# Kernel tuning notes

Hardware: AMD Instinct MI355X
Metric: run time of the kernel (lower is better)

## Reference

```python
import jax, jax.numpy as jnp
import numpy as np

VOCAB = 256
PAD = 0
D_MODEL = 512
ATTN_DIM = 64
B, L = 8, 2048
LN_EPS = 1e-5


def layer_norm(x, g, b):
    mu = jnp.mean(x, axis=-1, keepdims=True)
    var = jnp.mean(jnp.square(x - mu), axis=-1, keepdims=True)
    return (x - mu) * jax.lax.rsqrt(var + LN_EPS) * g + b


def setup_inputs() -> dict:
    key = jax.random.key(0)
    ks = jax.random.split(key, 10)
    tokens = jax.random.randint(ks[0], (B, L), 1, VOCAB)  # avoid PAD=0
    prefix_lens = jax.random.randint(ks[1], (B,), 256, 1536)
    embed_w = jax.random.normal(ks[2], (VOCAB, D_MODEL), jnp.float32) * 0.02
    embed_w = embed_w.at[PAD].set(0.0)  # padding_idx row
    en_g = jnp.ones((D_MODEL,), jnp.float32)
    en_b = jnp.zeros((D_MODEL,), jnp.float32)
    fn_g = jnp.ones((D_MODEL,), jnp.float32)
    fn_b = jnp.zeros((D_MODEL,), jnp.float32)
    q_w = jax.random.normal(ks[3], (ATTN_DIM, D_MODEL), jnp.float32) * 0.02
    q_b = jnp.zeros((ATTN_DIM,), jnp.float32)
    k_w = jax.random.normal(ks[4], (ATTN_DIM, D_MODEL), jnp.float32) * 0.02
    k_b = jnp.zeros((ATTN_DIM,), jnp.float32)
    g_w = jax.random.normal(ks[5], (1, D_MODEL), jnp.float32) * 0.02
    g_b = jnp.full((1,), 2.0, jnp.float32)  # gate bias init to 2.0
    return dict(tokens=tokens, prefix_lens=prefix_lens, embed_w=embed_w,
                en_g=en_g, en_b=en_b, fn_g=fn_g, fn_b=fn_b,
                q_w=q_w, q_b=q_b, k_w=k_w, k_b=k_b, g_w=g_w, g_b=g_b)


def reference(tokens, prefix_lens, embed_w, en_g, en_b, fn_g, fn_b,
              q_w, q_b, k_w, k_b, g_w, g_b):
    # encode (n_layers=0: embed -> embed_norm -> final_norm)
    x = embed_w[tokens]                       # (B, L, D)
    x = layer_norm(x, en_g, en_b)
    h = layer_norm(x, fn_g, fn_b)

    vocab_logits = jnp.einsum('bld,vd->blv', h, embed_w)   # tied head
    q = h @ q_w.T + q_b                       # (B, L, A)
    k = h @ k_w.T + k_b                       # (B, L, A)
    scores = jnp.einsum('btd,bsd->bts', q, k) / np.sqrt(ATTN_DIM).astype(np.float32)

    idx = jnp.arange(L)[None, :]              # (1, L)
    prefix_mask = (idx < prefix_lens[:, None]) & (tokens != PAD)  # (B, L)
    scores = jnp.where(prefix_mask[:, None, :], scores, -jnp.inf)
    attn = jax.nn.softmax(scores, axis=-1)    # (B, L, L)

    prefix_onehot = jax.nn.one_hot(tokens, VOCAB, dtype=jnp.float32)
    prefix_onehot = prefix_onehot * prefix_mask[..., None]
    copy_dist = jnp.einsum('bts,bsv->btv', attn, prefix_onehot)  # (B, L, V)

    gate = jax.nn.sigmoid(h @ g_w.T + g_b)    # (B, L, 1)
    vocab_probs = jax.nn.softmax(vocab_logits, axis=-1)
    mixed = gate * vocab_probs + (1.0 - gate) * copy_dist
    mixed = jnp.clip(mixed, 1e-12, None)
    return jnp.log(mixed), gate[..., 0], attn
```

## Files before the change

### kernel.cpp

```cpp
#include <hip/hip_runtime.h>
#include <math.h>


#define DM 512
#define VC 256
#define SL 2048
#define NB 8
#define AD 64

typedef float f4v __attribute__((ext_vector_type(4)));

__device__ __forceinline__ float wave_sum(float v) {
#pragma unroll
  for (int o = 32; o > 0; o >>= 1) v += __shfl_xor(v, o, 64);
  return v;
}
__device__ __forceinline__ float wave_max(float v) {
#pragma unroll
  for (int o = 32; o > 0; o >>= 1) v = fmaxf(v, __shfl_xor(v, o, 64));
  return v;
}
__device__ __forceinline__ float blk_sum(float v, float* red) {
  v = wave_sum(v);
  if ((threadIdx.x & 63) == 0) red[threadIdx.x >> 6] = v;
  __syncthreads();
  float r = red[0] + red[1] + red[2] + red[3];
  __syncthreads();
  return r;
}
__device__ __forceinline__ float blk_max(float v, float* red) {
  v = wave_max(v);
  if ((threadIdx.x & 63) == 0) red[threadIdx.x >> 6] = v;
  __syncthreads();
  float r = fmaxf(fmaxf(red[0], red[1]), fmaxf(red[2], red[3]));
  __syncthreads();
  return r;
}

__global__ __launch_bounds__(256) void kprep(
    const float* __restrict__ embed_w, const float* __restrict__ q_w,
    const float* __restrict__ k_w, const int* __restrict__ tokens,
    const int* __restrict__ prefix_lens,
    float* __restrict__ embed_P, float* __restrict__ qk_P,
    int* __restrict__ cnt)
{
  __shared__ int c[VC];
  const int blk = blockIdx.x;
  const int tid = threadIdx.x;
  if (blk < DM) {
    const int d = blk;
    embed_P[(((d >> 2) * VC + tid) << 2) + (d & 3)] = embed_w[tid * DM + d];
    if (tid < 128) {
      float val = (tid < 64) ? q_w[tid * DM + d] : k_w[(tid - 64) * DM + d];
      qk_P[(((d >> 2) * 128 + tid) << 2) + (d & 3)] = val;
    }
  } else {
    const int b = blk - DM;
    c[tid] = 0;
    __syncthreads();
    const int P = prefix_lens[b];
    const int4* trow = (const int4*)(tokens + b * SL);
#pragma unroll
    for (int i = tid; i < SL / 4; i += 256) {
      int4 tk = trow[i];
      int s0 = i * 4;
      if (s0     < P && tk.x != 0) atomicAdd(&c[tk.x], 1);
      if (s0 + 1 < P && tk.y != 0) atomicAdd(&c[tk.y], 1);
      if (s0 + 2 < P && tk.z != 0) atomicAdd(&c[tk.z], 1);
      if (s0 + 3 < P && tk.w != 0) atomicAdd(&c[tk.w], 1);
    }
    __syncthreads();
    cnt[b * VC + tid] = c[tid];
  }
}

__global__ __launch_bounds__(256) void ktok(
    const float* __restrict__ embed_w,
    const float* __restrict__ en_g, const float* __restrict__ en_b,
    const float* __restrict__ fn_g, const float* __restrict__ fn_b,
    const float* __restrict__ q_b, const float* __restrict__ k_b,
    const float* __restrict__ g_w, const float* __restrict__ g_b,
    const float* __restrict__ embed_P, const float* __restrict__ qk_P,
    float* __restrict__ q_tok, float* __restrict__ kT_P,
    float* __restrict__ gate_tok, float* __restrict__ probs_tok)
{
  __shared__ float red[4];
  __shared__ __align__(16) float hs[DM];
  const int tt = blockIdx.x;
  const int tid = threadIdx.x;

  float x0 = embed_w[tt * DM + tid];
  float x1 = embed_w[tt * DM + 256 + tid];
  float mu = blk_sum(x0 + x1, red) * (1.0f / DM);
  float d0 = x0 - mu, d1 = x1 - mu;
  float var = blk_sum(d0 * d0 + d1 * d1, red) * (1.0f / DM);
  float inv = 1.0f / sqrtf(var + 1e-5f);
  float y0 = d0 * inv * en_g[tid] + en_b[tid];
  float y1 = d1 * inv * en_g[tid + 256] + en_b[tid + 256];
  mu = blk_sum(y0 + y1, red) * (1.0f / DM);
  d0 = y0 - mu; d1 = y1 - mu;
  var = blk_sum(d0 * d0 + d1 * d1, red) * (1.0f / DM);
  inv = 1.0f / sqrtf(var + 1e-5f);
  float h0 = d0 * inv * fn_g[tid] + fn_b[tid];
  float h1 = d1 * inv * fn_g[tid + 256] + fn_b[tid + 256];
  hs[tid] = h0; hs[tid + 256] = h1;
  float gp = blk_sum(h0 * g_w[tid] + h1 * g_w[tid + 256], red);
  if (tid == 0) gate_tok[tt] = 1.0f / (1.0f + expf(-(gp + g_b[0])));

  const float4* hs4 = (const float4*)hs;
  const float4* w4p = (const float4*)qk_P;
  const float4* e4p = (const float4*)embed_P;
  const bool qk_lane = (tid < 128);
  float acc = 0.0f;
  float lt = 0.0f;
#pragma unroll 8
  for (int d4 = 0; d4 < DM / 4; ++d4) {
    float4 h4 = hs4[d4];
    float4 e4 = e4p[d4 * VC + tid];
    lt += h4.x * e4.x + h4.y * e4.y + h4.z * e4.z + h4.w * e4.w;
    if (qk_lane) {
      float4 w4 = w4p[d4 * 128 + tid];
      acc += h4.x * w4.x + h4.y * w4.y + h4.z * w4.z + h4.w * w4.w;
    }
  }
  if (qk_lane) {
    if (tid < 64) {
      q_tok[tt * AD + tid] = acc + q_b[tid];
    } else {
      int a = tid - 64;
      kT_P[(((a >> 2) * VC + tt) << 2) + (a & 3)] = acc + k_b[a];
    }
  }
  float m = blk_max(lt, red);
  float e = expf(lt - m);
  float Z = blk_sum(e, red);
  probs_tok[tt * VC + tid] = e / Z;
}

__global__ __launch_bounds__(256) void ktables(
    const float* __restrict__ q_tok, const float* __restrict__ kT_P,
    const int* __restrict__ cnt, const float* __restrict__ gate_tok,
    const float* __restrict__ probs_tok,
    float* __restrict__ e_norm, float* __restrict__ logmix)
{
  __shared__ float red[4];
  __shared__ __align__(16) float qs[AD];
  const int b = blockIdx.x >> 8, tt = blockIdx.x & 255;
  const int v = threadIdx.x;
  if (v < AD) qs[v] = q_tok[tt * AD + v];
  __syncthreads();
  const float4* qs4 = (const float4*)qs;
  const float4* k4p = (const float4*)kT_P;
  float sv = 0.0f;
#pragma unroll
  for (int a4 = 0; a4 < AD / 4; ++a4) {
    float4 q4 = qs4[a4];
    float4 k4 = k4p[a4 * VC + v];
    sv += q4.x * k4.x + q4.y * k4.y + q4.z * k4.z + q4.w * k4.w;
  }
  sv *= 0.125f;
  int c = cnt[b * VC + v];
  float m = blk_max(c > 0 ? sv : -1e30f, red);
  float e = expf(sv - m);
  float Z = blk_sum((float)c * e, red);
  float en = e / Z;
  int idx = (b * VC + tt) * VC + v;
  e_norm[idx] = en;
  float g = gate_tok[tt];
  float mixed = g * probs_tok[tt * VC + v] + (1.0f - g) * ((float)c * en);
  logmix[idx] = logf(fmaxf(mixed, 1e-12f));
}

__global__ __launch_bounds__(256) void kwrite(
    const int* __restrict__ tokens, const int* __restrict__ prefix_lens,
    const float* __restrict__ e_norm, const float* __restrict__ logmix,
    const float* __restrict__ gate_tok,
    float* __restrict__ out_logmix, float* __restrict__ out_gate,
    float* __restrict__ out_attn)
{
  __shared__ float erow[VC];
  const int row = blockIdx.x;
  const int b = row >> 11;
  const int tid = threadIdx.x;
  const int P = prefix_lens[b];
  const int4* tokrow = (const int4*)(tokens + b * SL);
  int4 tk0 = tokrow[tid];
  int4 tk1 = tokrow[tid + 256];
  const int tt = tokens[row];
  const int base = (b * VC + tt) * VC;
  erow[tid] = e_norm[base + tid];
  __builtin_nontemporal_store(logmix[base + tid],
                              &out_logmix[(size_t)row * VC + tid]);
  if (tid == 0) out_gate[row] = gate_tok[tt];
  __syncthreads();
  f4v* arow = (f4v*)(out_attn + (size_t)row * SL);
  {
    int s0 = tid * 4;
    f4v val;
    val.x = (s0     < P && tk0.x != 0) ? erow[tk0.x] : 0.0f;
    val.y = (s0 + 1 < P && tk0.y != 0) ? erow[tk0.y] : 0.0f;
    val.z = (s0 + 2 < P && tk0.z != 0) ? erow[tk0.z] : 0.0f;
    val.w = (s0 + 3 < P && tk0.w != 0) ? erow[tk0.w] : 0.0f;
    __builtin_nontemporal_store(val, &arow[tid]);
  }
  {
    int s0 = (tid + 256) * 4;
    f4v val;
    val.x = (s0     < P && tk1.x != 0) ? erow[tk1.x] : 0.0f;
    val.y = (s0 + 1 < P && tk1.y != 0) ? erow[tk1.y] : 0.0f;
    val.z = (s0 + 2 < P && tk1.z != 0) ? erow[tk1.z] : 0.0f;
    val.w = (s0 + 3 < P && tk1.w != 0) ? erow[tk1.w] : 0.0f;
    __builtin_nontemporal_store(val, &arow[tid + 256]);
  }
}

extern "C" void kernel_launch(void* const* d_in, const int* in_sizes, int n_in,
                              void* d_out, int out_size, void* d_ws, size_t ws_size,
                              hipStream_t stream)
{
  const int*   tokens      = (const int*)  d_in[0];
  const int*   prefix_lens = (const int*)  d_in[1];
  const float* embed_w     = (const float*)d_in[2];
  const float* en_g        = (const float*)d_in[3];
  const float* en_b        = (const float*)d_in[4];
  const float* fn_g        = (const float*)d_in[5];
  const float* fn_b        = (const float*)d_in[6];
  const float* q_b         = (const float*)d_in[8];
  const float* k_b         = (const float*)d_in[10];
  const float* q_w         = (const float*)d_in[7];
  const float* k_w         = (const float*)d_in[9];
  const float* g_w         = (const float*)d_in[11];
  const float* g_b         = (const float*)d_in[12];

  float* ws        = (float*)d_ws;
  float* embed_P   = ws;
  float* qk_P      = embed_P + DM * VC;
  float* kT_P      = qk_P + DM * 128;
  float* q_tok     = kT_P + AD * VC;
  float* gate_tok  = q_tok + VC * AD;
  float* probs_tok = gate_tok + VC;
  int*   cnt       = (int*)(probs_tok + VC * VC);
  float* e_norm    = (float*)(cnt + NB * VC);
  float* logmix    = e_norm + NB * VC * VC;

  float* out_logmix = (float*)d_out;
  float* out_gate   = out_logmix + (size_t)NB * SL * VC;
  float* out_attn   = out_gate + (size_t)NB * SL;

  kprep<<<DM + NB, 256, 0, stream>>>(embed_w, q_w, k_w, tokens, prefix_lens,
                                     embed_P, qk_P, cnt);
  ktok<<<VC, 256, 0, stream>>>(embed_w, en_g, en_b, fn_g, fn_b, q_b, k_b,
                               g_w, g_b, embed_P, qk_P,
                               q_tok, kT_P, gate_tok, probs_tok);
  ktables<<<NB * VC, 256, 0, stream>>>(q_tok, kT_P, cnt, gate_tok, probs_tok,
                                       e_norm, logmix);
  kwrite<<<NB * SL, 256, 0, stream>>>(tokens, prefix_lens, e_norm, logmix,
                                      gate_tok, out_logmix, out_gate, out_attn);
}
```

Measured before the change: 239.8 us.

## Fuse table and write kernels via per-token row lists built by counting sort

kprep now also counts every token occurrence per batch, prefix-sums the counts and scatters row positions into per-(batch,token) lists. A single fused kernel per (batch, token) computes the attention and log-mix rows once, then writes them directly to every output row holding that token. This removes the e_norm/logmix workspace round-trip and a separate 16K-block launch. Write work is now unevenly spread across blocks according to token frequency, and output writes are scattered rather than sequential.

Result: no change. 238.5 us, median of 2 (-0.5%).

```diff
diff --git a/kernel.cpp b/kernel.cpp
--- a/kernel.cpp
+++ b/kernel.cpp
@@ -42,9 +42,13 @@
     const float* __restrict__ k_w, const int* __restrict__ tokens,
     const int* __restrict__ prefix_lens,
     float* __restrict__ embed_P, float* __restrict__ qk_P,
-    int* __restrict__ cnt)
+    int* __restrict__ cnt, int* __restrict__ ncnt,
+    int* __restrict__ offs, int* __restrict__ list)
 {
   __shared__ int c[VC];
+  __shared__ int ca[VC];
+  __shared__ int off[VC];
+  __shared__ int cur[VC];
   const int blk = blockIdx.x;
   const int tid = threadIdx.x;
   if (blk < DM) {
@@ -56,7 +60,7 @@
     }
   } else {
     const int b = blk - DM;
-    c[tid] = 0;
+    c[tid] = 0; ca[tid] = 0;
     __syncthreads();
     const int P = prefix_lens[b];
     const int4* trow = (const int4*)(tokens + b * SL);
@@ -64,13 +68,40 @@
     for (int i = tid; i < SL / 4; i += 256) {
       int4 tk = trow[i];
       int s0 = i * 4;
+      atomicAdd(&ca[tk.x], 1); atomicAdd(&ca[tk.y], 1);
+      atomicAdd(&ca[tk.z], 1); atomicAdd(&ca[tk.w], 1);
       if (s0     < P && tk.x != 0) atomicAdd(&c[tk.x], 1);
       if (s0 + 1 < P && tk.y != 0) atomicAdd(&c[tk.y], 1);
       if (s0 + 2 < P && tk.z != 0) atomicAdd(&c[tk.z], 1);
       if (s0 + 3 < P && tk.w != 0) atomicAdd(&c[tk.w], 1);
     }
     __syncthreads();
-    cnt[b * VC + tid] = c[tid];
+    int myc = ca[tid];
+    off[tid] = myc;
+    __syncthreads();
+    for (int d2 = 1; d2 < VC; d2 <<= 1) {
+      int add = (tid >= d2) ? off[tid - d2] : 0;
+      __syncthreads();
+      off[tid] += add;
+      __syncthreads();
+    }
+    int excl = off[tid] - myc;
+    cur[tid] = excl;
+    __syncthreads();
+#pragma unroll
+    for (int i = tid; i < SL / 4; i += 256) {
+      int4 tk = trow[i];
+      int s0 = i * 4;
+      int p;
+      p = atomicAdd(&cur[tk.x], 1); list[b * SL + p] = s0;
+      p = atomicAdd(&cur[tk.y], 1); list[b * SL + p] = s0 + 1;
+      p = atomicAdd(&cur[tk.z], 1); list[b * SL + p] = s0 + 2;
+      p = atomicAdd(&cur[tk.w], 1); list[b * SL + p] = s0 + 3;
+    }
+    __syncthreads();
+    cnt [b * VC + tid] = c[tid];
+    ncnt[b * VC + tid] = myc;
+    offs[b * VC + tid] = excl;
   }
 }
 
@@ -137,80 +168,76 @@
   probs_tok[tt * VC + tid] = e / Z;
 }
 
-__global__ __launch_bounds__(256) void ktables(
+__global__ __launch_bounds__(256) void kfused(
     const float* __restrict__ q_tok, const float* __restrict__ kT_P,
-    const int* __restrict__ cnt, const float* __restrict__ gate_tok,
-    const float* __restrict__ probs_tok,
-    float* __restrict__ e_norm, float* __restrict__ logmix)
+    const int* __restrict__ cnt, const int* __restrict__ ncnt,
+    const int* __restrict__ offs, const int* __restrict__ list,
+    const float* __restrict__ gate_tok, const float* __restrict__ probs_tok,
+    const int* __restrict__ tokens, const int* __restrict__ prefix_lens,
+    float* __restrict__ out_logmix, float* __restrict__ out_gate,
+    float* __restrict__ out_attn)
 {
   __shared__ float red[4];
   __shared__ __align__(16) float qs[AD];
+  __shared__ __align__(16) float erow[VC];
   const int b = blockIdx.x >> 8, tt = blockIdx.x & 255;
-  const int v = threadIdx.x;
-  if (v < AD) qs[v] = q_tok[tt * AD + v];
-  __syncthreads();
+  const int tid = threadIdx.x;
+
+  const int P = prefix_lens[b];
+  const int4* tokrow = (const int4*)(tokens + b * SL);
+  int4 tk0 = tokrow[tid];
+  int4 tk1 = tokrow[tid + 256];
+  const int nr = ncnt[b * VC + tt];
+  const int base_off = offs[b * VC + tt];
+  const float pv = probs_tok[tt * VC + tid];
+  const float g = gate_tok[tt];
+  if (tid < AD) qs[tid] = q_tok[tt * AD + tid];
+  __syncthreads();
+
   const float4* qs4 = (const float4*)qs;
   const float4* k4p = (const float4*)kT_P;
   float sv = 0.0f;
 #pragma unroll
   for (int a4 = 0; a4 < AD / 4; ++a4) {
     float4 q4 = qs4[a4];
-    float4 k4 = k4p[a4 * VC + v];
+    float4 k4 = k4p[a4 * VC + tid];
     sv += q4.x * k4.x + q4.y * k4.y + q4.z * k4.z + q4.w * k4.w;
   }
   sv *= 0.125f;
-  int c = cnt[b * VC + v];
+  int c = cnt[b * VC + tid];
   float m = blk_max(c > 0 ? sv : -1e30f, red);
   float e = expf(sv - m);
   float Z = blk_sum((float)c * e, red);
   float en = e / Z;
-  int idx = (b * VC + tt) * VC + v;
-  e_norm[idx] = en;
-  float g = gate_tok[tt];
-  float mixed = g * probs_tok[tt * VC + v] + (1.0f - g) * ((float)c * en);
-  logmix[idx] = logf(fmaxf(mixed, 1e-12f));
-}
-
-__global__ __launch_bounds__(256) void kwrite(
-    const int* __restrict__ tokens, const int* __restrict__ prefix_lens,
-    const float* __restrict__ e_norm, const float* __restrict__ logmix,
-    const float* __restrict__ gate_tok,
-    float* __restrict__ out_logmix, float* __restrict__ out_gate,
-    float* __restrict__ out_attn)
-{
-  __shared__ float erow[VC];
-  const int row = blockIdx.x;
-  const int b = row >> 11;
-  const int tid = threadIdx.x;
-  const int P = prefix_lens[b];
-  const int4* tokrow = (const int4*)(tokens + b * SL);
-  int4 tk0 = tokrow[tid];
-  int4 tk1 = tokrow[tid + 256];
-  const int tt = tokens[row];
-  const int base = (b * VC + tt) * VC;
-  erow[tid] = e_norm[base + tid];
-  __builtin_nontemporal_store(logmix[base + tid],
-                              &out_logmix[(size_t)row * VC + tid]);
-  if (tid == 0) out_gate[row] = gate_tok[tt];
-  __syncthreads();
-  f4v* arow = (f4v*)(out_attn + (size_t)row * SL);
+  erow[tid] = en;
+  float lv = logf(fmaxf(g * pv + (1.0f - g) * ((float)c * en), 1e-12f));
+  __syncthreads();
+
+  f4v a0, a1;
   {
     int s0 = tid * 4;
-    f4v val;
-    val.x = (s0     < P && tk0.x != 0) ? erow[tk0.x] : 0.0f;
-    val.y = (s0 + 1 < P && tk0.y != 0) ? erow[tk0.y] : 0.0f;
-    val.z = (s0 + 2 < P && tk0.z != 0) ? erow[tk0.z] : 0.0f;
-    val.w = (s0 + 3 < P && tk0.w != 0) ? erow[tk0.w] : 0.0f;
-    __builtin_nontemporal_store(val, &arow[tid]);
+    a0.x = (s0     < P && tk0.x != 0) ? erow[tk0.x] : 0.0f;
+    a0.y = (s0 + 1 < P && tk0.y != 0) ? erow[tk0.y] : 0.0f;
+    a0.z = (s0 + 2 < P && tk0.z != 0) ? erow[tk0.z] : 0.0f;
+    a0.w = (s0 + 3 < P && tk0.w != 0) ? erow[tk0.w] : 0.0f;
   }
   {
     int s0 = (tid + 256) * 4;
-    f4v val;
-    val.x = (s0     < P && tk1.x != 0) ? erow[tk1.x] : 0.0f;
-    val.y = (s0 + 1 < P && tk1.y != 0) ? erow[tk1.y] : 0.0f;
-    val.z = (s0 + 2 < P && tk1.z != 0) ? erow[tk1.z] : 0.0f;
-    val.w = (s0 + 3 < P && tk1.w != 0) ? erow[tk1.w] : 0.0f;
-    __builtin_nontemporal_store(val, &arow[tid + 256]);
+    a1.x = (s0     < P && tk1.x != 0) ? erow[tk1.x] : 0.0f;
+    a1.y = (s0 + 1 < P && tk1.y != 0) ? erow[tk1.y] : 0.0f;
+    a1.z = (s0 + 2 < P && tk1.z != 0) ? erow[tk1.z] : 0.0f;
+    a1.w = (s0 + 3 < P && tk1.w != 0) ? erow[tk1.w] : 0.0f;
+  }
+
+  const int* lp = list + b * SL + base_off;
+  for (int r = 0; r < nr; ++r) {
+    int t = lp[r];
+    size_t row = (size_t)(b * SL + t);
+    __builtin_nontemporal_store(lv, &out_logmix[row * VC + tid]);
+    if (tid == 0) out_gate[row] = g;
+    f4v* ar = (f4v*)(out_attn + row * SL);
+    __builtin_nontemporal_store(a0, &ar[tid]);
+    __builtin_nontemporal_store(a1, &ar[tid + 256]);
   }
 }
 
@@ -240,20 +267,20 @@
   float* gate_tok  = q_tok + VC * AD;
   float* probs_tok = gate_tok + VC;
   int*   cnt       = (int*)(probs_tok + VC * VC);
-  float* e_norm    = (float*)(cnt + NB * VC);
-  float* logmix    = e_norm + NB * VC * VC;
+  int*   ncnt      = cnt + NB * VC;
+  int*   offs      = ncnt + NB * VC;
+  int*   list      = offs + NB * VC;
 
   float* out_logmix = (float*)d_out;
   float* out_gate   = out_logmix + (size_t)NB * SL * VC;
   float* out_attn   = out_gate + (size_t)NB * SL;
 
   kprep<<<DM + NB, 256, 0, stream>>>(embed_w, q_w, k_w, tokens, prefix_lens,
-                                     embed_P, qk_P, cnt);
+                                     embed_P, qk_P, cnt, ncnt, offs, list);
   ktok<<<VC, 256, 0, stream>>>(embed_w, en_g, en_b, fn_g, fn_b, q_b, k_b,
                                g_w, g_b, embed_P, qk_P,
                                q_tok, kT_P, gate_tok, probs_tok);
-  ktables<<<NB * VC, 256, 0, stream>>>(q_tok, kT_P, cnt, gate_tok, probs_tok,
-                                       e_norm, logmix);
-  kwrite<<<NB * SL, 256, 0, stream>>>(tokens, prefix_lens, e_norm, logmix,
-                                      gate_tok, out_logmix, out_gate, out_attn);
-}
+  kfused<<<NB * VC, 256, 0, stream>>>(q_tok, kT_P, cnt, ncnt, offs, list,
+                                      gate_tok, probs_tok, tokens, prefix_lens,
+                                      out_logmix, out_gate, out_attn);
+}
```
